# Kernel tuning notes

Measured on AMD Instinct MI355X. Metric: run time of the kernel, lower is better.

## Reference

```python
import jax, jax.numpy as jnp
import numpy as np

N_SRC, N_DST, E, D, OUT = 100000, 20000, 600000, 128, 128

def setup_inputs() -> dict:
    key = jax.random.key(0)
    k1, k2, k3, k4, k5 = jax.random.split(key, 5)
    h = jax.random.normal(k1, (N_SRC, D), dtype=jnp.float32)
    edge_src = jax.random.randint(k2, (E,), 0, N_SRC, dtype=jnp.int64)
    edge_dst = jax.random.randint(k3, (E,), 0, N_DST, dtype=jnp.int64)
    W = jax.random.normal(k4, (OUT, 2 * D), dtype=jnp.float32) * (1.0 / np.sqrt(2 * D))
    b = jax.random.normal(k5, (OUT,), dtype=jnp.float32) * 0.01
    return {"h": h, "edge_src": edge_src, "edge_dst": edge_dst, "W": W, "b": b, "n_dst": N_DST}

def reference(h, edge_src, edge_dst, W, b, n_dst):
    # dst nodes are the first n_dst src nodes (DGL block convention)
    h_dst = h[:n_dst]                                   # [n_dst, D]
    msgs = h[edge_src]                                  # gather: [E, D]
    agg = jax.ops.segment_sum(msgs, edge_dst, num_segments=n_dst)   # [n_dst, D]
    deg = jax.ops.segment_sum(jnp.ones(edge_src.shape, h.dtype), edge_dst, num_segments=n_dst)
    h_neigh = agg / jnp.maximum(deg, 1.0)[:, None]      # mean; 0-degree -> 0
    z = jnp.concatenate([h_dst, h_neigh], axis=1)       # [n_dst, 2D]
    return jax.nn.relu(z @ W.T + b)                     # [n_dst, OUT]
```

## Files before the change

kernel.cpp:

```cpp
#include <hip/hip_runtime.h>

#define DFEAT 128
#define KDIM  256
#define CAP   128
#define WSTR  264

typedef __attribute__((ext_vector_type(8))) short bf16x8;
typedef __attribute__((ext_vector_type(4))) float f32x4;

__device__ __forceinline__ float bflo(unsigned int u) {
    union { unsigned int i; float f; } v; v.i = u << 16; return v.f;
}
__device__ __forceinline__ float bfhi(unsigned int u) {
    union { unsigned int i; float f; } v; v.i = u & 0xffff0000u; return v.f;
}
__device__ __forceinline__ unsigned short f2bf(float f) {
    union { float f; unsigned int i; } v; v.f = f;
    unsigned int r = (v.i + 0x7fffu + ((v.i >> 16) & 1u)) >> 16;
    return (unsigned short)r;
}
__device__ __forceinline__ unsigned int pack2(float x, float y) {
    return ((unsigned int)f2bf(y) << 16) | (unsigned int)f2bf(x);
}
__device__ __forceinline__ uint4 cvt8(const float* p) {
    float4 a = *(const float4*)p;
    float4 b = *(const float4*)(p + 4);
    return make_uint4(pack2(a.x, a.y), pack2(a.z, a.w),
                      pack2(b.x, b.y), pack2(b.z, b.w));
}

__global__ __launch_bounds__(256) void prep_kernel(
    const float* __restrict__ h, const float* __restrict__ W,
    const int* __restrict__ esrc, const int* __restrict__ edst,
    unsigned short* __restrict__ hbf,
    unsigned short* __restrict__ z,
    unsigned short* __restrict__ Wbf,
    int* __restrict__ cnt, int* __restrict__ sorted,
    int E, int n_chunks, int B_C, int B_H, int cshift)
{
    int blk = blockIdx.x;
    int tid = threadIdx.x;
    if (blk < B_C) {
        int e0 = blk * 1024 + tid;
        int d[4], s[4];
        bool ok[4];
        #pragma unroll
        for (int r = 0; r < 4; ++r) {
            int e = e0 + r * 256;
            ok[r] = (e < E);
            d[r] = ok[r] ? edst[e] : 0;
            s[r] = ok[r] ? esrc[e] : 0;
        }
        int pos[4];
        #pragma unroll
        for (int r = 0; r < 4; ++r)
            pos[r] = ok[r] ? atomicAdd(&cnt[(size_t)d[r] << cshift], 1) : CAP;
        #pragma unroll
        for (int r = 0; r < 4; ++r)
            if (ok[r] && pos[r] < CAP)
                sorted[(size_t)d[r] * CAP + pos[r]] = s[r];
    } else if (blk < B_C + B_H) {
        int c0 = (blk - B_C) * 1024 + tid;
        #pragma unroll
        for (int r = 0; r < 4; ++r) {
            int t = c0 + r * 256;
            if (t < n_chunks) {
                uint4 v = cvt8(h + (size_t)t * 8);
                if (hbf) {
                    *(uint4*)(hbf + (size_t)t * 8) = v;
                } else {
                    int row = t >> 4;
                    int col = (t & 15) * 8;
                    *(uint4*)(z + (size_t)row * KDIM + col) = v;
                }
            }
        }
    } else {
        int t = (blk - B_C - B_H) * 256 + tid;
        *(uint4*)(Wbf + (size_t)t * 8) = cvt8(W + (size_t)t * 8);
    }
}

__global__ __launch_bounds__(256) void agg_bf16_kernel(
    const unsigned short* __restrict__ hbf, const int* __restrict__ cnt,
    const int* __restrict__ sorted, unsigned short* __restrict__ zn, int n_dst,
    int cshift)
{
    int wave = threadIdx.x >> 6;
    int lane = threadIdx.x & 63;
    int grp  = lane >> 4;
    int l16  = lane & 15;
    int d = blockIdx.x * 16 + wave * 4 + grp;

    int c = (d < n_dst) ? cnt[(size_t)d << cshift] : 0;
    if (c > CAP) c = CAP;
    const int* seg = sorted + (size_t)d * CAP;

    float acc[8];
    #pragma unroll
    for (int j = 0; j < 8; ++j) acc[j] = 0.f;

    const uint4* hp = (const uint4*)hbf + l16;
    int i = 0;
    for (; i + 7 < c; i += 8) {
        int ix[8];
        #pragma unroll
        for (int r = 0; r < 8; ++r) ix[r] = seg[i + r];
        uint4 u[8];
        #pragma unroll
        for (int r = 0; r < 8; ++r) u[r] = hp[(size_t)ix[r] * 16];
        #pragma unroll
        for (int r = 0; r < 8; ++r) {
            acc[0] += bflo(u[r].x); acc[1] += bfhi(u[r].x);
            acc[2] += bflo(u[r].y); acc[3] += bfhi(u[r].y);
            acc[4] += bflo(u[r].z); acc[5] += bfhi(u[r].z);
            acc[6] += bflo(u[r].w); acc[7] += bfhi(u[r].w);
        }
    }
    for (; i + 1 < c; i += 2) {
        int i0 = seg[i], i1 = seg[i + 1];
        uint4 u0 = hp[(size_t)i0 * 16], u1 = hp[(size_t)i1 * 16];
        acc[0] += bflo(u0.x) + bflo(u1.x); acc[1] += bfhi(u0.x) + bfhi(u1.x);
        acc[2] += bflo(u0.y) + bflo(u1.y); acc[3] += bfhi(u0.y) + bfhi(u1.y);
        acc[4] += bflo(u0.z) + bflo(u1.z); acc[5] += bfhi(u0.z) + bfhi(u1.z);
        acc[6] += bflo(u0.w) + bflo(u1.w); acc[7] += bfhi(u0.w) + bfhi(u1.w);
    }
    for (; i < c; ++i) {
        uint4 u = hp[(size_t)seg[i] * 16];
        acc[0] += bflo(u.x); acc[1] += bfhi(u.x);
        acc[2] += bflo(u.y); acc[3] += bfhi(u.y);
        acc[4] += bflo(u.z); acc[5] += bfhi(u.z);
        acc[6] += bflo(u.w); acc[7] += bfhi(u.w);
    }
    float inv = 1.0f / fmaxf((float)c, 1.0f);
    if (d < n_dst)
        ((uint4*)zn)[(size_t)d * 16 + l16] = make_uint4(
            pack2(acc[0] * inv, acc[1] * inv), pack2(acc[2] * inv, acc[3] * inv),
            pack2(acc[4] * inv, acc[5] * inv), pack2(acc[6] * inv, acc[7] * inv));
}

__global__ __launch_bounds__(256) void agg_f32_kernel(
    const float* __restrict__ h, const int* __restrict__ cnt,
    const int* __restrict__ sorted, unsigned short* __restrict__ z, int n_dst,
    int cshift)
{
    int d = blockIdx.x * 4 + (threadIdx.x >> 6);
    if (d >= n_dst) return;
    int lane = threadIdx.x & 63;
    int c = cnt[(size_t)d << cshift]; if (c > CAP) c = CAP;
    const int* seg = sorted + (size_t)d * CAP;
    float ax = 0.f, ay = 0.f;
    const float2* hp = (const float2*)h + lane;
    int i = 0;
    for (; i + 1 < c; i += 2) {
        int i0 = seg[i], i1 = seg[i + 1];
        float2 v0 = hp[(size_t)i0 * 64], v1 = hp[(size_t)i1 * 64];
        ax += v0.x + v1.x; ay += v0.y + v1.y;
    }
    for (; i < c; ++i) {
        float2 v = hp[(size_t)seg[i] * 64];
        ax += v.x; ay += v.y;
    }
    float inv = 1.0f / fmaxf((float)c, 1.0f);
    ((unsigned int*)z)[(size_t)d * 128 + 64 + lane] = pack2(ax * inv, ay * inv);
}

__global__ __launch_bounds__(256) void gemm_kernel(
    const unsigned short* __restrict__ alo, int slo,
    const unsigned short* __restrict__ ahi, int shi,
    const unsigned short* __restrict__ Wbf,
    const float* __restrict__ bias,
    float* __restrict__ out,
    int n_dst)
{
    __shared__ unsigned short Wl[DFEAT][WSTR];

    int tid  = threadIdx.x;
    int wave = tid >> 6;
    int lane = tid & 63;
    int quad = lane >> 4;
    int l16  = lane & 15;
    int m0   = blockIdx.x * 64 + wave * 16;

    #pragma unroll
    for (int i = 0; i < 16; ++i) {
        int u  = i * 256 + tid;
        int n  = u >> 5;
        int kq = (u & 31) * 8;
        *(uint4*)&Wl[n][kq] = *(const uint4*)(Wbf + (size_t)n * KDIM + kq);
    }

    int m_a = m0 + l16;
    if (m_a > n_dst - 1) m_a = n_dst - 1;

    f32x4 acc[8];
    #pragma unroll
    for (int ct = 0; ct < 8; ++ct) acc[ct] = (f32x4){0.f, 0.f, 0.f, 0.f};

    const unsigned short* plo = alo + (size_t)m_a * slo + quad * 8;
    const unsigned short* phi = ahi + (size_t)m_a * shi + quad * 8;

    __syncthreads();

    #pragma unroll
    for (int ks = 0; ks < 8; ++ks) {
        bf16x8 a = (ks < 4) ? *(const bf16x8*)(plo + ks * 32)
                            : *(const bf16x8*)(phi + (ks - 4) * 32);
        #pragma unroll
        for (int ct = 0; ct < 8; ++ct) {
            bf16x8 bb = *(const bf16x8*)&Wl[ct * 16 + l16][ks * 32 + quad * 8];
            acc[ct] = __builtin_amdgcn_mfma_f32_16x16x32_bf16(a, bb, acc[ct], 0, 0, 0);
        }
    }

    #pragma unroll
    for (int ct = 0; ct < 8; ++ct) {
        int n = ct * 16 + l16;
        float bc = bias[n];
        #pragma unroll
        for (int r = 0; r < 4; ++r) {
            int m = m0 + quad * 4 + r;
            if (m < n_dst)
                out[(size_t)m * DFEAT + n] = fmaxf(acc[ct][r] + bc, 0.0f);
        }
    }
}


extern "C" void kernel_launch(void* const* d_in, const int* in_sizes, int n_in,
                              void* d_out, int out_size, void* d_ws, size_t ws_size,
                              hipStream_t stream) {
    const float* h  = (const float*)d_in[0];
    const int* esrc = (const int*)d_in[1];
    const int* edst = (const int*)d_in[2];
    const float* W  = (const float*)d_in[3];
    const float* b  = (const float*)d_in[4];
    float* out      = (float*)d_out;

    const int E     = in_sizes[1];
    const int n_src = in_sizes[0] / DFEAT;
    const int n_dst = out_size / DFEAT;

    size_t hbf_bytes  = (size_t)n_src * DFEAT * 2;
    size_t zn_bytes   = (size_t)n_dst * DFEAT * 2;
    size_t wbf_bytes  = (size_t)DFEAT * KDIM * 2;
    size_t cnt_base   = (size_t)n_dst * sizeof(int);
    size_t srt_bytes  = (size_t)n_dst * CAP * sizeof(int);

    int cshift = 5;
    bool fast;
    for (;;) {
        size_t cb = cnt_base << cshift;
        fast = ws_size >= hbf_bytes + zn_bytes + wbf_bytes + cb + srt_bytes;
        if (fast || cshift == 0) break;
        --cshift;
    }
    if (!fast) {
        cshift = 5;
        while (cshift > 0 &&
               ws_size < wbf_bytes + (cnt_base << cshift) + srt_bytes)
            --cshift;
    }
    size_t cnt_bytes = cnt_base << cshift;

    char* p = (char*)d_ws;
    unsigned short *hbf, *zn, *Wbf;
    int *cnt, *sorted;
    if (fast) {
        hbf = (unsigned short*)p;            p += hbf_bytes;
        zn  = (unsigned short*)p;            p += zn_bytes;
        Wbf = (unsigned short*)p;            p += wbf_bytes;
        cnt = (int*)p;                       p += cnt_bytes;
        sorted = (int*)p;
    } else {
        hbf = nullptr; zn = nullptr;
        Wbf = (unsigned short*)p;            p += wbf_bytes;
        cnt = (int*)p;                       p += cnt_bytes;
        sorted = (int*)p;
    }

    unsigned short* z = (unsigned short*)d_out;

    (void)hipMemsetAsync(cnt, 0, cnt_bytes, stream);

    int n_chunks = (fast ? n_src : n_dst) * (DFEAT / 8);
    int B_C = (E + 1023) / 1024;
    int B_H = (n_chunks + 1023) / 1024;
    int B_W = (DFEAT * KDIM / 8) / 256;
    prep_kernel<<<B_C + B_H + B_W, 256, 0, stream>>>(
        h, W, esrc, edst, hbf, fast ? nullptr : z, Wbf, cnt, sorted,
        E, n_chunks, B_C, B_H, cshift);

    if (fast) {
        agg_bf16_kernel<<<(n_dst + 15) / 16, 256, 0, stream>>>(
            hbf, cnt, sorted, zn, n_dst, cshift);
        gemm_kernel<<<(n_dst + 63) / 64, 256, 0, stream>>>(
            hbf, DFEAT, zn, DFEAT, Wbf, b, out, n_dst);
    } else {
        agg_f32_kernel<<<(n_dst + 3) / 4, 256, 0, stream>>>(
            h, cnt, sorted, z, n_dst, cshift);
        gemm_kernel<<<(n_dst + 63) / 64, 256, 0, stream>>>(
            z, KDIM, z + DFEAT, KDIM, Wbf, b, out, n_dst);
    }
}
```

Measured before the change: 172.1 us.

## Bin edges by source range and aggregate per-shard partials for gather locality

Edges are bucketed per destination into 8 source-index bins. Separate blocks aggregate each bin, with the bin in the low bits of the block index, so that concurrently running blocks gather from a narrower slice of the bf16 feature table and hit L2 better. Per-bin bf16 partial sums go to a new workspace buffer, and an extra finalize kernel sums them and divides by the degree. This costs more atomic counters, extra partial-buffer traffic, one more launch, bf16 rounding of the partials, and a 32-edges-per-bin cap that could drop edges under skew.

```diff
diff --git a/kernel.cpp b/kernel.cpp
--- a/kernel.cpp
+++ b/kernel.cpp
@@ -2,7 +2,9 @@
 
 #define DFEAT 128
 #define KDIM  256
-#define CAP   128
+#define NBIN  8
+#define BCAP  32
+#define CAP   256
 #define WSTR  264
 
 typedef __attribute__((ext_vector_type(8))) short bf16x8;
@@ -36,13 +38,13 @@
     unsigned short* __restrict__ z,
     unsigned short* __restrict__ Wbf,
     int* __restrict__ cnt, int* __restrict__ sorted,
-    int E, int n_chunks, int B_C, int B_H, int cshift)
+    int E, int n_chunks, int B_C, int B_H, int cshift, float rbinw)
 {
     int blk = blockIdx.x;
     int tid = threadIdx.x;
     if (blk < B_C) {
         int e0 = blk * 1024 + tid;
-        int d[4], s[4];
+        int d[4], s[4], bn[4];
         bool ok[4];
         #pragma unroll
         for (int r = 0; r < 4; ++r) {
@@ -50,15 +52,19 @@
             ok[r] = (e < E);
             d[r] = ok[r] ? edst[e] : 0;
             s[r] = ok[r] ? esrc[e] : 0;
+            int b = (int)((float)s[r] * rbinw);
+            bn[r] = (b > NBIN - 1) ? NBIN - 1 : b;
         }
         int pos[4];
         #pragma unroll
         for (int r = 0; r < 4; ++r)
-            pos[r] = ok[r] ? atomicAdd(&cnt[(size_t)d[r] << cshift], 1) : CAP;
+            pos[r] = ok[r]
+                ? atomicAdd(&cnt[(size_t)(d[r] * NBIN + bn[r]) << cshift], 1)
+                : BCAP;
         #pragma unroll
         for (int r = 0; r < 4; ++r)
-            if (ok[r] && pos[r] < CAP)
-                sorted[(size_t)d[r] * CAP + pos[r]] = s[r];
+            if (ok[r] && pos[r] < BCAP)
+                sorted[(size_t)d[r] * CAP + bn[r] * BCAP + pos[r]] = s[r];
     } else if (blk < B_C + B_H) {
         int c0 = (blk - B_C) * 1024 + tid;
         #pragma unroll
@@ -81,20 +87,23 @@
     }
 }
 
-__global__ __launch_bounds__(256) void agg_bf16_kernel(
+__global__ __launch_bounds__(256) void agg_part_kernel(
     const unsigned short* __restrict__ hbf, const int* __restrict__ cnt,
-    const int* __restrict__ sorted, unsigned short* __restrict__ zn, int n_dst,
-    int cshift)
-{
+    const int* __restrict__ sorted, unsigned short* __restrict__ part,
+    int n_dst, int cshift)
+{
+    int shard = blockIdx.x & (NBIN - 1);
+    int dblk  = blockIdx.x >> 3;
     int wave = threadIdx.x >> 6;
     int lane = threadIdx.x & 63;
     int grp  = lane >> 4;
     int l16  = lane & 15;
-    int d = blockIdx.x * 16 + wave * 4 + grp;
-
-    int c = (d < n_dst) ? cnt[(size_t)d << cshift] : 0;
-    if (c > CAP) c = CAP;
-    const int* seg = sorted + (size_t)d * CAP;
+    int d = dblk * 16 + wave * 4 + grp;
+    int dv = (d < n_dst) ? d : 0;
+
+    int c = (d < n_dst) ? cnt[(size_t)(dv * NBIN + shard) << cshift] : 0;
+    if (c > BCAP) c = BCAP;
+    const int* seg = sorted + (size_t)dv * CAP + shard * BCAP;
 
     float acc[8];
     #pragma unroll
@@ -102,28 +111,19 @@
 
     const uint4* hp = (const uint4*)hbf + l16;
     int i = 0;
-    for (; i + 7 < c; i += 8) {
-        int ix[8];
-        #pragma unroll
-        for (int r = 0; r < 8; ++r) ix[r] = seg[i + r];
-        uint4 u[8];
-        #pragma unroll
-        for (int r = 0; r < 8; ++r) u[r] = hp[(size_t)ix[r] * 16];
-        #pragma unroll
-        for (int r = 0; r < 8; ++r) {
-            acc[0] += bflo(u[r].x); acc[1] += bfhi(u[r].x);
-            acc[2] += bflo(u[r].y); acc[3] += bfhi(u[r].y);
-            acc[4] += bflo(u[r].z); acc[5] += bfhi(u[r].z);
-            acc[6] += bflo(u[r].w); acc[7] += bfhi(u[r].w);
-        }
-    }
-    for (; i + 1 < c; i += 2) {
-        int i0 = seg[i], i1 = seg[i + 1];
+    for (; i + 3 < c; i += 4) {
+        int i0 = seg[i],     i1 = seg[i + 1];
+        int i2 = seg[i + 2], i3 = seg[i + 3];
         uint4 u0 = hp[(size_t)i0 * 16], u1 = hp[(size_t)i1 * 16];
-        acc[0] += bflo(u0.x) + bflo(u1.x); acc[1] += bfhi(u0.x) + bfhi(u1.x);
-        acc[2] += bflo(u0.y) + bflo(u1.y); acc[3] += bfhi(u0.y) + bfhi(u1.y);
-        acc[4] += bflo(u0.z) + bflo(u1.z); acc[5] += bfhi(u0.z) + bfhi(u1.z);
-        acc[6] += bflo(u0.w) + bflo(u1.w); acc[7] += bfhi(u0.w) + bfhi(u1.w);
+        uint4 u2 = hp[(size_t)i2 * 16], u3 = hp[(size_t)i3 * 16];
+        acc[0] += bflo(u0.x) + bflo(u1.x) + bflo(u2.x) + bflo(u3.x);
+        acc[1] += bfhi(u0.x) + bfhi(u1.x) + bfhi(u2.x) + bfhi(u3.x);
+        acc[2] += bflo(u0.y) + bflo(u1.y) + bflo(u2.y) + bflo(u3.y);
+        acc[3] += bfhi(u0.y) + bfhi(u1.y) + bfhi(u2.y) + bfhi(u3.y);
+        acc[4] += bflo(u0.z) + bflo(u1.z) + bflo(u2.z) + bflo(u3.z);
+        acc[5] += bfhi(u0.z) + bfhi(u1.z) + bfhi(u2.z) + bfhi(u3.z);
+        acc[6] += bflo(u0.w) + bflo(u1.w) + bflo(u2.w) + bflo(u3.w);
+        acc[7] += bfhi(u0.w) + bfhi(u1.w) + bfhi(u2.w) + bfhi(u3.w);
     }
     for (; i < c; ++i) {
         uint4 u = hp[(size_t)seg[i] * 16];
@@ -132,11 +132,35 @@
         acc[4] += bflo(u.z); acc[5] += bfhi(u.z);
         acc[6] += bflo(u.w); acc[7] += bfhi(u.w);
     }
-    float inv = 1.0f / fmaxf((float)c, 1.0f);
     if (d < n_dst)
-        ((uint4*)zn)[(size_t)d * 16 + l16] = make_uint4(
-            pack2(acc[0] * inv, acc[1] * inv), pack2(acc[2] * inv, acc[3] * inv),
-            pack2(acc[4] * inv, acc[5] * inv), pack2(acc[6] * inv, acc[7] * inv));
+        ((uint4*)part)[((size_t)shard * n_dst + d) * 16 + l16] = make_uint4(
+            pack2(acc[0], acc[1]), pack2(acc[2], acc[3]),
+            pack2(acc[4], acc[5]), pack2(acc[6], acc[7]));
+}
+
+__global__ __launch_bounds__(256) void agg_fin_kernel(
+    const int* __restrict__ cnt, const unsigned short* __restrict__ part,
+    unsigned short* __restrict__ zn, int n_dst, int cshift)
+{
+    int d = blockIdx.x * 4 + (threadIdx.x >> 6);
+    if (d >= n_dst) return;
+    int lane = threadIdx.x & 63;
+
+    int tot = 0;
+    #pragma unroll
+    for (int x = 0; x < NBIN; ++x) {
+        int c = cnt[(size_t)(d * NBIN + x) << cshift];
+        tot += (c > BCAP) ? BCAP : c;
+    }
+    float lo = 0.f, hi = 0.f;
+    #pragma unroll
+    for (int x = 0; x < NBIN; ++x) {
+        unsigned int u =
+            ((const unsigned int*)part)[((size_t)x * n_dst + d) * 64 + lane];
+        lo += bflo(u); hi += bfhi(u);
+    }
+    float inv = 1.0f / fmaxf((float)tot, 1.0f);
+    ((unsigned int*)zn)[(size_t)d * 64 + lane] = pack2(lo * inv, hi * inv);
 }
 
 __global__ __launch_bounds__(256) void agg_f32_kernel(
@@ -147,21 +171,20 @@
     int d = blockIdx.x * 4 + (threadIdx.x >> 6);
     if (d >= n_dst) return;
     int lane = threadIdx.x & 63;
-    int c = cnt[(size_t)d << cshift]; if (c > CAP) c = CAP;
-    const int* seg = sorted + (size_t)d * CAP;
     float ax = 0.f, ay = 0.f;
+    int tot = 0;
     const float2* hp = (const float2*)h + lane;
-    int i = 0;
-    for (; i + 1 < c; i += 2) {
-        int i0 = seg[i], i1 = seg[i + 1];
-        float2 v0 = hp[(size_t)i0 * 64], v1 = hp[(size_t)i1 * 64];
-        ax += v0.x + v1.x; ay += v0.y + v1.y;
-    }
-    for (; i < c; ++i) {
-        float2 v = hp[(size_t)seg[i] * 64];
-        ax += v.x; ay += v.y;
-    }
-    float inv = 1.0f / fmaxf((float)c, 1.0f);
+    for (int b = 0; b < NBIN; ++b) {
+        int c = cnt[(size_t)(d * NBIN + b) << cshift];
+        if (c > BCAP) c = BCAP;
+        tot += c;
+        const int* seg = sorted + (size_t)d * CAP + b * BCAP;
+        for (int i = 0; i < c; ++i) {
+            float2 v = hp[(size_t)seg[i] * 64];
+            ax += v.x; ay += v.y;
+        }
+    }
+    float inv = 1.0f / fmaxf((float)tot, 1.0f);
     ((unsigned int*)z)[(size_t)d * 128 + 64 + lane] = pack2(ax * inv, ay * inv);
 }
 
@@ -244,19 +267,21 @@
     size_t hbf_bytes  = (size_t)n_src * DFEAT * 2;
     size_t zn_bytes   = (size_t)n_dst * DFEAT * 2;
     size_t wbf_bytes  = (size_t)DFEAT * KDIM * 2;
-    size_t cnt_base   = (size_t)n_dst * sizeof(int);
+    size_t part_bytes = (size_t)NBIN * n_dst * DFEAT * 2;
+    size_t cnt_base   = (size_t)n_dst * NBIN * sizeof(int);
     size_t srt_bytes  = (size_t)n_dst * CAP * sizeof(int);
 
-    int cshift = 5;
+    int cshift = 4;
     bool fast;
     for (;;) {
         size_t cb = cnt_base << cshift;
-        fast = ws_size >= hbf_bytes + zn_bytes + wbf_bytes + cb + srt_bytes;
+        fast = ws_size >=
+               hbf_bytes + zn_bytes + wbf_bytes + part_bytes + cb + srt_bytes;
         if (fast || cshift == 0) break;
         --cshift;
     }
     if (!fast) {
-        cshift = 5;
+        cshift = 4;
         while (cshift > 0 &&
                ws_size < wbf_bytes + (cnt_base << cshift) + srt_bytes)
             --cshift;
@@ -264,36 +289,44 @@
     size_t cnt_bytes = cnt_base << cshift;
 
     char* p = (char*)d_ws;
-    unsigned short *hbf, *zn, *Wbf;
+    unsigned short *hbf, *zn, *Wbf, *part;
     int *cnt, *sorted;
     if (fast) {
-        hbf = (unsigned short*)p;            p += hbf_bytes;
-        zn  = (unsigned short*)p;            p += zn_bytes;
+        hbf  = (unsigned short*)p;           p += hbf_bytes;
+        zn   = (unsigned short*)p;           p += zn_bytes;
+        Wbf  = (unsigned short*)p;           p += wbf_bytes;
+        part = (unsigned short*)p;           p += part_bytes;
+        cnt  = (int*)p;                      p += cnt_bytes;
+        sorted = (int*)p;
+    } else {
+        hbf = nullptr; zn = nullptr; part = nullptr;
         Wbf = (unsigned short*)p;            p += wbf_bytes;
         cnt = (int*)p;                       p += cnt_bytes;
         sorted = (int*)p;
-    } else {
-        hbf = nullptr; zn = nullptr;
-        Wbf = (unsigned short*)p;            p += wbf_bytes;
-        cnt = (int*)p;                       p += cnt_bytes;
-        sorted = (int*)p;
     }
 
     unsigned short* z = (unsigned short*)d_out;
 
     (void)hipMemsetAsync(cnt, 0, cnt_bytes, stream);
+
+    int binw = (n_src + NBIN - 1) / NBIN;
+    float rbinw = 1.0f / (float)binw;
 
     int n_chunks = (fast ? n_src : n_dst) * (DFEAT / 8);
     int B_C = (E + 1023) / 1024;
     int B_H = (n_chunks + 1023) / 1024;
     int B_W = (DFEAT * KDIM / 8) / 256;
+
     prep_kernel<<<B_C + B_H + B_W, 256, 0, stream>>>(
         h, W, esrc, edst, hbf, fast ? nullptr : z, Wbf, cnt, sorted,
-        E, n_chunks, B_C, B_H, cshift);
+        E, n_chunks, B_C, B_H, cshift, rbinw);
 
     if (fast) {
-        agg_bf16_kernel<<<(n_dst + 15) / 16, 256, 0, stream>>>(
-            hbf, cnt, sorted, zn, n_dst, cshift);
+        int B_A = NBIN * ((n_dst + 15) / 16);
+        agg_part_kernel<<<B_A, 256, 0, stream>>>(
+            hbf, cnt, sorted, part, n_dst, cshift);
+        agg_fin_kernel<<<(n_dst + 3) / 4, 256, 0, stream>>>(
+            cnt, part, zn, n_dst, cshift);
         gemm_kernel<<<(n_dst + 63) / 64, 256, 0, stream>>>(
             hbf, DFEAT, zn, DFEAT, Wbf, b, out, n_dst);
     } else {
```

Result: slower. 181.2 us (+5.3%).
